# Performance work log

Hardware: AMD Instinct MI355X
Metric: run time of the kernel (lower is better)

Reference implementation:

```python
import jax, jax.numpy as jnp
import numpy as np

B, F0, D = 2048, 39, 16
CROSS = [200, 200, 200]


def setup_inputs() -> dict:
    key = jax.random.key(0)
    ks = jax.random.split(key, 7)
    inp = {"x": jax.random.normal(ks[0], (B, F0, D), dtype=jnp.float32)}
    prev = F0
    for i, c in enumerate(CROSS):
        # Conv1d(in=F0*prev, out=c, kernel=1) weight reshaped to (c, F0, prev)
        scale = 1.0 / np.sqrt(F0 * prev)
        inp[f"W{i}"] = jax.random.normal(ks[1 + 2 * i], (c, F0, prev), dtype=jnp.float32) * scale
        inp[f"b{i}"] = jnp.zeros((c,), dtype=jnp.float32)
        prev = c
    return inp


def reference(x, W0, b0, W1, b1, W2, b2):
    # x: (B, F0, D). Each CIN layer in torch materializes x0*h -> (B, F0*prev, D)
    # then applies a kernel-1 Conv1d. Mathematically this is the bilinear
    # contraction below (same values, no quadratic intermediate).
    x0 = x
    h = x
    xs = []
    for W, b in ((W0, b0), (W1, b1), (W2, b2)):
        # z[b,o,d] = sum_{f,g} W[o,f,g] * x0[b,f,d] * h[b,g,d] + bias[o]
        z = jnp.einsum('bfd,bgd,ofg->bod', x0, h, W) + b[None, :, None]
        h = jax.nn.relu(z)
        xs.append(h)
    # concat over channel dim, sum-pool over embed dim -> (B, sum(cross_sizes))
    return jnp.sum(jnp.concatenate(xs, axis=1), axis=2)
```

## Files before the change

### kernel.cpp

```cpp
#include <hip/hip_runtime.h>
#include <hip/hip_bf16.h>
#include <stdint.h>

typedef __attribute__((ext_vector_type(8))) short bf16x8;
typedef __attribute__((ext_vector_type(4))) float f32x4;
typedef __attribute__((ext_vector_type(16))) float f32x16;
typedef unsigned short u16;
typedef unsigned int u32;

#define GLL(gp, lp) __builtin_amdgcn_global_load_lds( \
    (const __attribute__((address_space(1))) void*)(gp), \
    (__attribute__((address_space(3))) void*)(lp), 16, 0, 0)

__device__ __forceinline__ u16 f2bf_rne(float v) {
    u32 u = __float_as_uint(v);
    u32 r = (u + 0x7fffu + ((u >> 16) & 1u)) >> 16;
    return (u16)r;
}


__global__ void pack_x_kernel(const float* __restrict__ x, u16* __restrict__ xbd) {
    int idx = blockIdx.x * 256 + threadIdx.x;
    if (idx >= 32768 * 40) return;
    int m = idx / 40, f = idx - m * 40;
    int b = m >> 4, d = m & 15;
    float v = (f < 39) ? x[(b * 39 + f) * 16 + d] : 0.0f;
    xbd[idx] = f2bf_rne(v);
}

template <int LAYER>
__global__ void pack_wfrag_kernel(const float* __restrict__ W, u16* __restrict__ Wpk) {
    constexpr int TOT = (LAYER == 0) ? 401408 : 1835008;
    int idx = blockIdx.x * 256 + threadIdx.x;
    if (idx >= TOT) return;
    int j = idx & 7;
    int lane = (idx >> 3) & 63;
    int rest = idx >> 9;
    int nt = rest % 7, ks = rest / 7;
    int o = nt * 32 + (lane & 31);
    int k = ks * 16 + ((lane >> 5) << 3) + j;
    float v = 0.0f;
    if constexpr (LAYER == 0) {
        int f = k / 40, g = k - f * 40;
        if (o < 200 && f < 39 && g < 39) v = W[(o * 39 + f) * 39 + g];
    } else {
        int f = k / 208, g = k - f * 208;
        if (o < 200 && f < 39 && g < 200) v = W[o * 7800 + f * 200 + g];
    }
    Wpk[idx] = f2bf_rne(v);
}

template <int LAYER>
__global__ __launch_bounds__(512, 2) void cin_gemm6(
    const u16* __restrict__ Xbd,
    const u16* __restrict__ Hin,
    const u16* __restrict__ Bpk,
    const float* __restrict__ bias,
    u16* __restrict__ Hout,
    float* __restrict__ out)
{
    constexpr int KP    = (LAYER == 0) ? 1792 : 8192;
    constexpr int NITER = KP / 64;
    constexpr u32 MAGIC = (LAYER == 0) ? 3277u : 10083u;
    constexpr int SHIFT = (LAYER == 0) ? 17 : 21;
    constexpr int GS    = (LAYER == 0) ? 40 : 208;
    constexpr int GCL   = (LAYER == 0) ? 32 : 200;
    constexpr int HROW  = (LAYER == 0) ? 40 : 216;

    __shared__ __align__(16) char smem[114688];
    u16* Xl = (u16*)smem;
    u16* Hl = (u16*)(smem + 10240);

    const int bid  = blockIdx.x;
    const int m0   = bid * 128;
    const int tid  = threadIdx.x;
    const int lane = tid & 63, wid = tid >> 6;
    const int mg = wid & 1, kg = (wid >> 1) & 1, ng = wid >> 2;
    const int l31 = lane & 31, grp8 = lane >> 5;
    const int nt0 = ng * 4;
    const int NTW = ng ? 3 : 4;

    {
        const char* xsrc = (const char*)(Xbd + (size_t)m0 * 40);
        for (int i = wid; i < 10; i += 8)
            GLL(xsrc + i * 1024 + lane * 16, smem + i * 1024);
    }
    if constexpr (LAYER > 0) {
        const u16* hsrc = Hin + (size_t)m0 * 208;
        #pragma unroll
        for (int j = 0; j < 7; ++j) {
            int u = tid + j * 512;
            if (u < 3328) {
                int r = u / 26, q = u - r * 26;
                int4 v = *(const int4*)(hsrc + r * 208 + q * 8);
                *(int4*)(Hl + r * 216 + q * 8) = v;
            }
        }
    }

    int xrow40[2], hrow[2];
    #pragma unroll
    for (int sub = 0; sub < 2; ++sub) {
        int r = mg * 64 + sub * 32 + l31;
        xrow40[sub] = r * 40;
        hrow[sub]   = r * HROW;
    }
    const u16* Hb = (LAYER == 0) ? Xl : Hl;

    f32x16 acc[2][4];
    #pragma unroll
    for (int s = 0; s < 2; ++s)
        #pragma unroll
        for (int t = 0; t < 4; ++t)
            acc[s][t] = (f32x16){0,0,0,0,0,0,0,0,0,0,0,0,0,0,0,0};

    bf16x8 bA[2][4], bB[2][4];

#define LOADB2(it_, dst) { \
    _Pragma("unroll") \
    for (int s_ = 0; s_ < 2; ++s_) { \
        int ks_ = 4 * (it_) + 2 * kg + s_; \
        _Pragma("unroll") \
        for (int t_ = 0; t_ < 4; ++t_) \
            if (t_ < NTW) \
                dst[s_][t_] = *(const bf16x8*)(Bpk + (size_t)ks_ * 3584 + (nt0 + t_) * 512 + lane * 8); \
    } }

#define COMPUTE2(it_, src) { \
    _Pragma("unroll") \
    for (int s_ = 0; s_ < 2; ++s_) { \
        int ks_ = 4 * (it_) + 2 * kg + s_; \
        int k0_ = ks_ * 16 + grp8 * 8; \
        u32 f_ = ((u32)k0_ * MAGIC) >> SHIFT; \
        f_ = (f_ > 39u) ? 39u : f_; \
        int g0_ = k0_ - (int)f_ * GS; \
        g0_ = (g0_ > GCL) ? GCL : g0_; \
        _Pragma("unroll") \
        for (int sub_ = 0; sub_ < 2; ++sub_) { \
            u16 xs_ = Xl[xrow40[sub_] + (int)f_]; \
            bf16x8 hv_ = *(const bf16x8*)&Hb[hrow[sub_] + g0_]; \
            float xf_ = __uint_as_float(((u32)xs_) << 16); \
            union { bf16x8 v; u32 w[4]; } hu_, au_; \
            hu_.v = hv_; \
            _Pragma("unroll") \
            for (int j_ = 0; j_ < 4; ++j_) { \
                float lo_ = __uint_as_float(hu_.w[j_] << 16); \
                float hi_ = __uint_as_float(hu_.w[j_] & 0xffff0000u); \
                float pl_ = xf_ * lo_, ph_ = xf_ * hi_; \
                u32 pk_; \
                asm("v_cvt_pk_bf16_f32 %0, %1, %2" : "=v"(pk_) : "v"(pl_), "v"(ph_)); \
                au_.w[j_] = pk_; \
            } \
            bf16x8 af_ = au_.v; \
            _Pragma("unroll") \
            for (int t_ = 0; t_ < 4; ++t_) \
                if (t_ < NTW) \
                    acc[sub_][t_] = __builtin_amdgcn_mfma_f32_32x32x16_bf16(af_, src[s_][t_], acc[sub_][t_], 0, 0, 0); \
        } \
    } }

    LOADB2(0, bA);
    __syncthreads();

    for (int it = 0; it < NITER; it += 2) {
        LOADB2(it + 1, bB);
        COMPUTE2(it, bA);
        if (it + 2 < NITER) LOADB2(it + 2, bA);
        COMPUTE2(it + 1, bB);
    }
#undef LOADB2
#undef COMPUTE2

    __syncthreads();
    float* red = (float*)smem;
    if (kg == 1) {
        #pragma unroll
        for (int sub = 0; sub < 2; ++sub)
            #pragma unroll
            for (int t = 0; t < 4; ++t)
                if (t < NTW) {
                    int T = (mg * 2 + sub) * 7 + nt0 + t;
                    float* p = red + T * 1024 + lane * 16;
                    f32x16 a = acc[sub][t];
                    *(f32x4*)(p + 0)  = (f32x4){a[0], a[1], a[2], a[3]};
                    *(f32x4*)(p + 4)  = (f32x4){a[4], a[5], a[6], a[7]};
                    *(f32x4*)(p + 8)  = (f32x4){a[8], a[9], a[10], a[11]};
                    *(f32x4*)(p + 12) = (f32x4){a[12], a[13], a[14], a[15]};
                }
    }
    __syncthreads();

    if (kg == 0) {
        #pragma unroll
        for (int sub = 0; sub < 2; ++sub) {
            int rowbase = m0 + mg * 64 + sub * 32;
            int bA0 = rowbase >> 4;
            #pragma unroll
            for (int t = 0; t < 4; ++t) {
                if (t < NTW) {
                    int T = (mg * 2 + sub) * 7 + nt0 + t;
                    const float* p = red + T * 1024 + lane * 16;
                    f32x4 o0 = *(const f32x4*)(p + 0);
                    f32x4 o1 = *(const f32x4*)(p + 4);
                    f32x4 o2 = *(const f32x4*)(p + 8);
                    f32x4 o3 = *(const f32x4*)(p + 12);
                    int oc = nt0 * 32 + t * 32 + l31;
                    float bs = (oc < 200) ? bias[oc] : 0.0f;
                    f32x16 a = acc[sub][t];
                    float hv[16];
                    #pragma unroll
                    for (int r = 0; r < 4; ++r) {
                        hv[r]      = fmaxf(a[r]      + o0[r] + bs, 0.0f);
                        hv[r + 4]  = fmaxf(a[r + 4]  + o1[r] + bs, 0.0f);
                        hv[r + 8]  = fmaxf(a[r + 8]  + o2[r] + bs, 0.0f);
                        hv[r + 12] = fmaxf(a[r + 12] + o3[r] + bs, 0.0f);
                    }
                    if constexpr (LAYER < 2) {
                        if (oc < 208) {
                            #pragma unroll
                            for (int r = 0; r < 16; ++r) {
                                int rl = (r & 3) + 8 * (r >> 2) + 4 * grp8;
                                Hout[(size_t)(rowbase + rl) * 208 + oc] = f2bf_rne(hv[r]);
                            }
                        }
                    }
                    float sA = ((hv[0] + hv[1]) + (hv[2] + hv[3])) + ((hv[4] + hv[5]) + (hv[6] + hv[7]));
                    float sB = ((hv[8] + hv[9]) + (hv[10] + hv[11])) + ((hv[12] + hv[13]) + (hv[14] + hv[15]));
                    sA += __shfl_xor(sA, 32);
                    sB += __shfl_xor(sB, 32);
                    if (lane < 32 && oc < 200) {
                        out[(size_t)bA0 * 600 + LAYER * 200 + oc] = sA;
                        out[(size_t)(bA0 + 1) * 600 + LAYER * 200 + oc] = sB;
                    }
                }
            }
        }
    }
}

extern "C" void kernel_launch(void* const* d_in, const int* in_sizes, int n_in,
                              void* d_out, int out_size, void* d_ws, size_t ws_size,
                              hipStream_t stream) {
    const float* x  = (const float*)d_in[0];
    const float* W0 = (const float*)d_in[1];
    const float* b0 = (const float*)d_in[2];
    const float* W1 = (const float*)d_in[3];
    const float* b1 = (const float*)d_in[4];
    const float* W2 = (const float*)d_in[5];
    const float* b2 = (const float*)d_in[6];
    float* out = (float*)d_out;

    char* ws = (char*)d_ws;
    u16* xbd  = (u16*)(ws);
    u16* wpk0 = (u16*)(ws + 2622464);
    u16* wpk1 = (u16*)(ws + 3425280);
    u16* wpk2 = (u16*)(ws + 7095296);
    u16* h1   = (u16*)(ws + 10765312);
    u16* h2   = (u16*)(ws + 24397824);

    pack_x_kernel<<<5120, 256, 0, stream>>>(x, xbd);
    pack_wfrag_kernel<0><<<1568, 256, 0, stream>>>(W0, wpk0);
    pack_wfrag_kernel<1><<<7168, 256, 0, stream>>>(W1, wpk1);
    pack_wfrag_kernel<2><<<7168, 256, 0, stream>>>(W2, wpk2);

    cin_gemm6<0><<<256, 512, 0, stream>>>(xbd, xbd, wpk0, b0, h1, out);
    cin_gemm6<1><<<256, 512, 0, stream>>>(xbd, h1, wpk1, b1, h2, out);
    cin_gemm6<2><<<256, 512, 0, stream>>>(xbd, h2, wpk2, b2, (u16*)nullptr, out);
}
```

Measured before the change: 309.1 us.

## Split CIN GEMM blocks across N halves to double grid and occupancy

Each 128-row block is now split into two blocks that each cover half of the output channels (4 or 3 tiles of 32). The grid doubles to 512 blocks, shared memory drops to 64KB and launch bounds ask for 4 blocks per CU. Each wave now owns one 32-row group instead of two, and the B-fragment double buffering is removed in favour of a simple per-iteration load. The aim is more parallelism and occupancy, at the cost of building the bilinear A operand twice per row block and losing the explicit prefetch of B.

```diff
diff --git a/kernel.cpp b/kernel.cpp
--- a/kernel.cpp
+++ b/kernel.cpp
@@ -51,7 +51,7 @@
 }
 
 template <int LAYER>
-__global__ __launch_bounds__(512, 2) void cin_gemm6(
+__global__ __launch_bounds__(512, 4) void cin_gemm9(
     const u16* __restrict__ Xbd,
     const u16* __restrict__ Hin,
     const u16* __restrict__ Bpk,
@@ -67,18 +67,20 @@
     constexpr int GCL   = (LAYER == 0) ? 32 : 200;
     constexpr int HROW  = (LAYER == 0) ? 40 : 216;
 
-    __shared__ __align__(16) char smem[114688];
+    __shared__ __align__(16) char smem[65536];
     u16* Xl = (u16*)smem;
     u16* Hl = (u16*)(smem + 10240);
 
-    const int bid  = blockIdx.x;
-    const int m0   = bid * 128;
+    const int bid   = blockIdx.x;
+    const int mblk  = bid >> 1, nblk = bid & 1;
+    const int m0    = mblk * 128;
+    const int nbase = nblk * 128;
+    const int ntg0  = nblk * 4;
+    const int NTB   = nblk ? 3 : 4;
     const int tid  = threadIdx.x;
     const int lane = tid & 63, wid = tid >> 6;
-    const int mg = wid & 1, kg = (wid >> 1) & 1, ng = wid >> 2;
+    const int rg = wid & 3, kg = wid >> 2;
     const int l31 = lane & 31, grp8 = lane >> 5;
-    const int nt0 = ng * 4;
-    const int NTW = ng ? 3 : 4;
 
     {
         const char* xsrc = (const char*)(Xbd + (size_t)m0 * 40);
@@ -98,140 +100,113 @@
         }
     }
 
-    int xrow40[2], hrow[2];
+    const int rrow   = rg * 32 + l31;
+    const int xrow40 = rrow * 40;
+    const int hrow   = rrow * HROW;
+    const u16* Hb = (LAYER == 0) ? Xl : Hl;
+
+    f32x16 acc[4];
     #pragma unroll
-    for (int sub = 0; sub < 2; ++sub) {
-        int r = mg * 64 + sub * 32 + l31;
-        xrow40[sub] = r * 40;
-        hrow[sub]   = r * HROW;
-    }
-    const u16* Hb = (LAYER == 0) ? Xl : Hl;
-
-    f32x16 acc[2][4];
-    #pragma unroll
-    for (int s = 0; s < 2; ++s)
-        #pragma unroll
-        for (int t = 0; t < 4; ++t)
-            acc[s][t] = (f32x16){0,0,0,0,0,0,0,0,0,0,0,0,0,0,0,0};
-
-    bf16x8 bA[2][4], bB[2][4];
-
-#define LOADB2(it_, dst) { \
-    _Pragma("unroll") \
-    for (int s_ = 0; s_ < 2; ++s_) { \
-        int ks_ = 4 * (it_) + 2 * kg + s_; \
-        _Pragma("unroll") \
-        for (int t_ = 0; t_ < 4; ++t_) \
-            if (t_ < NTW) \
-                dst[s_][t_] = *(const bf16x8*)(Bpk + (size_t)ks_ * 3584 + (nt0 + t_) * 512 + lane * 8); \
-    } }
-
-#define COMPUTE2(it_, src) { \
-    _Pragma("unroll") \
-    for (int s_ = 0; s_ < 2; ++s_) { \
-        int ks_ = 4 * (it_) + 2 * kg + s_; \
-        int k0_ = ks_ * 16 + grp8 * 8; \
-        u32 f_ = ((u32)k0_ * MAGIC) >> SHIFT; \
-        f_ = (f_ > 39u) ? 39u : f_; \
-        int g0_ = k0_ - (int)f_ * GS; \
-        g0_ = (g0_ > GCL) ? GCL : g0_; \
-        _Pragma("unroll") \
-        for (int sub_ = 0; sub_ < 2; ++sub_) { \
-            u16 xs_ = Xl[xrow40[sub_] + (int)f_]; \
-            bf16x8 hv_ = *(const bf16x8*)&Hb[hrow[sub_] + g0_]; \
-            float xf_ = __uint_as_float(((u32)xs_) << 16); \
-            union { bf16x8 v; u32 w[4]; } hu_, au_; \
-            hu_.v = hv_; \
-            _Pragma("unroll") \
-            for (int j_ = 0; j_ < 4; ++j_) { \
-                float lo_ = __uint_as_float(hu_.w[j_] << 16); \
-                float hi_ = __uint_as_float(hu_.w[j_] & 0xffff0000u); \
-                float pl_ = xf_ * lo_, ph_ = xf_ * hi_; \
-                u32 pk_; \
-                asm("v_cvt_pk_bf16_f32 %0, %1, %2" : "=v"(pk_) : "v"(pl_), "v"(ph_)); \
-                au_.w[j_] = pk_; \
-            } \
-            bf16x8 af_ = au_.v; \
-            _Pragma("unroll") \
-            for (int t_ = 0; t_ < 4; ++t_) \
-                if (t_ < NTW) \
-                    acc[sub_][t_] = __builtin_amdgcn_mfma_f32_32x32x16_bf16(af_, src[s_][t_], acc[sub_][t_], 0, 0, 0); \
-        } \
-    } }
-
-    LOADB2(0, bA);
+    for (int t = 0; t < 4; ++t)
+        acc[t] = (f32x16){0,0,0,0,0,0,0,0,0,0,0,0,0,0,0,0};
+
     __syncthreads();
 
-    for (int it = 0; it < NITER; it += 2) {
-        LOADB2(it + 1, bB);
-        COMPUTE2(it, bA);
-        if (it + 2 < NITER) LOADB2(it + 2, bA);
-        COMPUTE2(it + 1, bB);
-    }
-#undef LOADB2
-#undef COMPUTE2
+    for (int it = 0; it < NITER; ++it) {
+        bf16x8 bA[2][4];
+        #pragma unroll
+        for (int s = 0; s < 2; ++s) {
+            int ks = 4 * it + 2 * kg + s;
+            const u16* bp = Bpk + (size_t)ks * 3584 + ntg0 * 512 + lane * 8;
+            #pragma unroll
+            for (int t = 0; t < 4; ++t)
+                if (t < NTB)
+                    bA[s][t] = *(const bf16x8*)(bp + t * 512);
+        }
+        #pragma unroll
+        for (int s = 0; s < 2; ++s) {
+            int ks = 4 * it + 2 * kg + s;
+            int k0 = ks * 16 + grp8 * 8;
+            u32 f = ((u32)k0 * MAGIC) >> SHIFT;
+            f = (f > 39u) ? 39u : f;
+            int g0 = k0 - (int)f * GS;
+            g0 = (g0 > GCL) ? GCL : g0;
+            u16 xs = Xl[xrow40 + (int)f];
+            bf16x8 hvv = *(const bf16x8*)&Hb[hrow + g0];
+            float xf = __uint_as_float(((u32)xs) << 16);
+            union { bf16x8 v; u32 w[4]; } hu, au;
+            hu.v = hvv;
+            #pragma unroll
+            for (int j = 0; j < 4; ++j) {
+                float lo = __uint_as_float(hu.w[j] << 16);
+                float hi = __uint_as_float(hu.w[j] & 0xffff0000u);
+                float pl = xf * lo, ph = xf * hi;
+                u32 pk;
+                asm("v_cvt_pk_bf16_f32 %0, %1, %2" : "=v"(pk) : "v"(pl), "v"(ph));
+                au.w[j] = pk;
+            }
+            bf16x8 af = au.v;
+            #pragma unroll
+            for (int t = 0; t < 4; ++t)
+                if (t < NTB)
+                    acc[t] = __builtin_amdgcn_mfma_f32_32x32x16_bf16(af, bA[s][t], acc[t], 0, 0, 0);
+        }
+    }
 
     __syncthreads();
     float* red = (float*)smem;
     if (kg == 1) {
         #pragma unroll
-        for (int sub = 0; sub < 2; ++sub)
-            #pragma unroll
-            for (int t = 0; t < 4; ++t)
-                if (t < NTW) {
-                    int T = (mg * 2 + sub) * 7 + nt0 + t;
-                    float* p = red + T * 1024 + lane * 16;
-                    f32x16 a = acc[sub][t];
-                    *(f32x4*)(p + 0)  = (f32x4){a[0], a[1], a[2], a[3]};
-                    *(f32x4*)(p + 4)  = (f32x4){a[4], a[5], a[6], a[7]};
-                    *(f32x4*)(p + 8)  = (f32x4){a[8], a[9], a[10], a[11]};
-                    *(f32x4*)(p + 12) = (f32x4){a[12], a[13], a[14], a[15]};
+        for (int t = 0; t < 4; ++t)
+            if (t < NTB) {
+                float* p = red + (rg * 4 + t) * 1024 + lane * 16;
+                f32x16 a = acc[t];
+                *(f32x4*)(p + 0)  = (f32x4){a[0], a[1], a[2], a[3]};
+                *(f32x4*)(p + 4)  = (f32x4){a[4], a[5], a[6], a[7]};
+                *(f32x4*)(p + 8)  = (f32x4){a[8], a[9], a[10], a[11]};
+                *(f32x4*)(p + 12) = (f32x4){a[12], a[13], a[14], a[15]};
+            }
+    }
+    __syncthreads();
+
+    if (kg == 0) {
+        const int rowbase = m0 + rg * 32;
+        const int bi0 = rowbase >> 4;
+        #pragma unroll
+        for (int t = 0; t < 4; ++t) {
+            if (t < NTB) {
+                const float* p = red + (rg * 4 + t) * 1024 + lane * 16;
+                f32x4 o0 = *(const f32x4*)(p + 0);
+                f32x4 o1 = *(const f32x4*)(p + 4);
+                f32x4 o2 = *(const f32x4*)(p + 8);
+                f32x4 o3 = *(const f32x4*)(p + 12);
+                int oc = nbase + t * 32 + l31;
+                float bs = (oc < 200) ? bias[oc] : 0.0f;
+                f32x16 a = acc[t];
+                float hv[16];
+                #pragma unroll
+                for (int r = 0; r < 4; ++r) {
+                    hv[r]      = fmaxf(a[r]      + o0[r] + bs, 0.0f);
+                    hv[r + 4]  = fmaxf(a[r + 4]  + o1[r] + bs, 0.0f);
+                    hv[r + 8]  = fmaxf(a[r + 8]  + o2[r] + bs, 0.0f);
+                    hv[r + 12] = fmaxf(a[r + 12] + o3[r] + bs, 0.0f);
                 }
-    }
-    __syncthreads();
-
-    if (kg == 0) {
-        #pragma unroll
-        for (int sub = 0; sub < 2; ++sub) {
-            int rowbase = m0 + mg * 64 + sub * 32;
-            int bA0 = rowbase >> 4;
-            #pragma unroll
-            for (int t = 0; t < 4; ++t) {
-                if (t < NTW) {
-                    int T = (mg * 2 + sub) * 7 + nt0 + t;
-                    const float* p = red + T * 1024 + lane * 16;
-                    f32x4 o0 = *(const f32x4*)(p + 0);
-                    f32x4 o1 = *(const f32x4*)(p + 4);
-                    f32x4 o2 = *(const f32x4*)(p + 8);
-                    f32x4 o3 = *(const f32x4*)(p + 12);
-                    int oc = nt0 * 32 + t * 32 + l31;
-                    float bs = (oc < 200) ? bias[oc] : 0.0f;
-                    f32x16 a = acc[sub][t];
-                    float hv[16];
-                    #pragma unroll
-                    for (int r = 0; r < 4; ++r) {
-                        hv[r]      = fmaxf(a[r]      + o0[r] + bs, 0.0f);
-                        hv[r + 4]  = fmaxf(a[r + 4]  + o1[r] + bs, 0.0f);
-                        hv[r + 8]  = fmaxf(a[r + 8]  + o2[r] + bs, 0.0f);
-                        hv[r + 12] = fmaxf(a[r + 12] + o3[r] + bs, 0.0f);
-                    }
-                    if constexpr (LAYER < 2) {
-                        if (oc < 208) {
-                            #pragma unroll
-                            for (int r = 0; r < 16; ++r) {
-                                int rl = (r & 3) + 8 * (r >> 2) + 4 * grp8;
-                                Hout[(size_t)(rowbase + rl) * 208 + oc] = f2bf_rne(hv[r]);
-                            }
+                if constexpr (LAYER < 2) {
+                    if (oc < 208) {
+                        #pragma unroll
+                        for (int r = 0; r < 16; ++r) {
+                            int rl = (r & 3) + 8 * (r >> 2) + 4 * grp8;
+                            Hout[(size_t)(rowbase + rl) * 208 + oc] = f2bf_rne(hv[r]);
                         }
                     }
-                    float sA = ((hv[0] + hv[1]) + (hv[2] + hv[3])) + ((hv[4] + hv[5]) + (hv[6] + hv[7]));
-                    float sB = ((hv[8] + hv[9]) + (hv[10] + hv[11])) + ((hv[12] + hv[13]) + (hv[14] + hv[15]));
-                    sA += __shfl_xor(sA, 32);
-                    sB += __shfl_xor(sB, 32);
-                    if (lane < 32 && oc < 200) {
-                        out[(size_t)bA0 * 600 + LAYER * 200 + oc] = sA;
-                        out[(size_t)(bA0 + 1) * 600 + LAYER * 200 + oc] = sB;
-                    }
+                }
+                float sA = ((hv[0] + hv[1]) + (hv[2] + hv[3])) + ((hv[4] + hv[5]) + (hv[6] + hv[7]));
+                float sB = ((hv[8] + hv[9]) + (hv[10] + hv[11])) + ((hv[12] + hv[13]) + (hv[14] + hv[15]));
+                sA += __shfl_xor(sA, 32);
+                sB += __shfl_xor(sB, 32);
+                if (lane < 32 && oc < 200) {
+                    out[(size_t)bi0 * 600 + LAYER * 200 + oc] = sA;
+                    out[(size_t)(bi0 + 1) * 600 + LAYER * 200 + oc] = sB;
                 }
             }
         }
@@ -263,7 +238,7 @@
     pack_wfrag_kernel<1><<<7168, 256, 0, stream>>>(W1, wpk1);
     pack_wfrag_kernel<2><<<7168, 256, 0, stream>>>(W2, wpk2);
 
-    cin_gemm6<0><<<256, 512, 0, stream>>>(xbd, xbd, wpk0, b0, h1, out);
-    cin_gemm6<1><<<256, 512, 0, stream>>>(xbd, h1, wpk1, b1, h2, out);
-    cin_gemm6<2><<<256, 512, 0, stream>>>(xbd, h2, wpk2, b2, (u16*)nullptr, out);
-}
+    cin_gemm9<0><<<512, 512, 0, stream>>>(xbd, xbd, wpk0, b0, h1, out);
+    cin_gemm9<1><<<512, 512, 0, stream>>>(xbd, h1, wpk1, b1, h2, out);
+    cin_gemm9<2><<<512, 512, 0, stream>>>(xbd, h2, wpk2, b2, (u16*)nullptr, out);
+}
```

Result: slower. 394.3 us (+27.6%).
